# Kernel tuning notes

Hardware: AMD Instinct MI355X
Metric: run time of the kernel (lower is better)

## Reference

```python
import jax, jax.numpy as jnp
import numpy as np

N_NODES = 100000
N_EDGES = 2400000


def setup_inputs() -> dict:
    key = jax.random.key(0)
    ks = jax.random.split(key, 6)
    x = jax.random.normal(ks[0], (N_NODES, 2), dtype=jnp.float32)
    edge_index = jax.random.randint(ks[1], (2, N_EDGES), 0, N_NODES, dtype=jnp.int64)
    # GCNConv weights (glorot-ish scale) and zero biases
    W1 = jax.random.normal(ks[2], (2, 32), dtype=jnp.float32) * (1.0 / np.sqrt(2.0))
    b1 = jnp.zeros((32,), dtype=jnp.float32)
    W2 = jax.random.normal(ks[3], (32, 32), dtype=jnp.float32) * (1.0 / np.sqrt(32.0))
    b2 = jnp.zeros((32,), dtype=jnp.float32)
    W3 = jax.random.normal(ks[4], (32, 1), dtype=jnp.float32) * (1.0 / np.sqrt(32.0))
    b3 = jnp.zeros((1,), dtype=jnp.float32)
    return {"x": x, "edge_index": edge_index, "W1": W1, "b1": b1,
            "W2": W2, "b2": b2, "W3": W3, "b3": b3}


def reference(x, edge_index, W1, b1, W2, b2, W3, b3):
    N = x.shape[0]
    self_loops = jnp.arange(N, dtype=edge_index.dtype)
    src = jnp.concatenate([edge_index[0], self_loops])  # message sources
    dst = jnp.concatenate([edge_index[1], self_loops])  # aggregation targets
    # Symmetric GCN normalization: deg computed at target nodes (PyG gcn_norm)
    deg = jax.ops.segment_sum(jnp.ones_like(dst, dtype=x.dtype), dst, num_segments=N)
    dinv = jnp.where(deg > 0, jax.lax.rsqrt(deg), 0.0)
    norm = (dinv[src] * dinv[dst])[:, None]  # [E+N, 1]

    def gcn_layer(h, W, b):
        h = h @ W                                  # [N, out]
        msg = norm * h[src]                        # gather + scale
        agg = jax.ops.segment_sum(msg, dst, num_segments=N)  # scatter-add
        return agg + b

    h = jax.nn.relu(gcn_layer(x, W1, b1))
    h = jax.nn.relu(gcn_layer(h, W2, b2))
    out = gcn_layer(h, W3, b3)
    return out.reshape(-1)
```

## Files before the change

### kernel.cpp

```cpp
#include <hip/hip_runtime.h>

#define NN 100000
#define NE 2400000
#define NB 391
#define CAP 6912
#define EPB 4096
#define NBLK2 ((NE + EPB - 1) / EPB)

__device__ __forceinline__ int wexscan(int v, int lane) {
    int x = v;
#pragma unroll
    for (int off = 1; off < 64; off <<= 1) {
        int t = __shfl_up(x, off, 64);
        x += (lane >= off) ? t : 0;
    }
    return x - v;
}

__global__ __launch_bounds__(512) void k_hist(const int* __restrict__ ei,
        int* __restrict__ bh) {
    __shared__ int hist[NB];
    int tid = threadIdx.x;
    for (int i = tid; i < NB; i += 512) hist[i] = 0;
    __syncthreads();
    int base_e = blockIdx.x * EPB + tid * 8;
    if (base_e + 8 <= NE) {
        int4 da = *(const int4*)(ei + NE + base_e);
        int4 db = *(const int4*)(ei + NE + base_e + 4);
        atomicAdd(&hist[da.x >> 8], 1); atomicAdd(&hist[da.y >> 8], 1);
        atomicAdd(&hist[da.z >> 8], 1); atomicAdd(&hist[da.w >> 8], 1);
        atomicAdd(&hist[db.x >> 8], 1); atomicAdd(&hist[db.y >> 8], 1);
        atomicAdd(&hist[db.z >> 8], 1); atomicAdd(&hist[db.w >> 8], 1);
    }
    __syncthreads();
    for (int i = tid; i < NB; i += 512) bh[blockIdx.x * NB + i] = hist[i];
}

__global__ __launch_bounds__(256) void k_offscan(int* __restrict__ bh,
        int* __restrict__ tot) {
    __shared__ int wsum[4];
    int b = blockIdx.x, tid = threadIdx.x;
    int lane = tid & 63, wid = tid >> 6;
    int carry = 0;
#pragma unroll
    for (int r = 0; r < 3; ++r) {
        int blk = r * 256 + tid;
        int v = (blk < NBLK2) ? bh[blk * NB + b] : 0;
        int ex = wexscan(v, lane);
        if (lane == 63) wsum[wid] = ex + v;
        __syncthreads();
        int woff = 0, rt = 0;
#pragma unroll
        for (int i = 0; i < 4; ++i) {
            woff += (i < wid) ? wsum[i] : 0;
            rt += wsum[i];
        }
        if (blk < NBLK2) bh[blk * NB + b] = b * CAP + carry + woff + ex;
        carry += rt;
        __syncthreads();
    }
    if (tid == 0) tot[b] = carry;
}

__global__ __launch_bounds__(512) void k_scatter2(const int* __restrict__ ei,
        const int* __restrict__ bh, int* __restrict__ binned) {
    __shared__ int hist[NB], lbase[NB], myb[NB];
    __shared__ int stage[EPB];
    __shared__ unsigned short stageb[EPB];
    __shared__ int wsum[8];
    int tid = threadIdx.x;
    for (int i = tid; i < NB; i += 512) {
        hist[i] = 0;
        myb[i] = bh[blockIdx.x * NB + i];
    }
    __syncthreads();
    int base_e = blockIdx.x * EPB + tid * 8;
    int pk[8], bn[8], rk[8];
    if (base_e + 8 <= NE) {
        const int4* s4 = (const int4*)(ei + base_e);
        const int4* d4 = (const int4*)(ei + NE + base_e);
        int4 sa = s4[0], sb = s4[1], da = d4[0], db = d4[1];
        int ss[8] = {sa.x, sa.y, sa.z, sa.w, sb.x, sb.y, sb.z, sb.w};
        int dd[8] = {da.x, da.y, da.z, da.w, db.x, db.y, db.z, db.w};
#pragma unroll
        for (int k = 0; k < 8; ++k) {
            bn[k] = dd[k] >> 8;
            pk[k] = ss[k] | ((dd[k] & 255) << 17);
            rk[k] = atomicAdd(&hist[bn[k]], 1);
        }
    } else {
#pragma unroll
        for (int k = 0; k < 8; ++k) bn[k] = -1;
    }
    __syncthreads();
    int lane = tid & 63, wid = tid >> 6;
    int v = (tid < NB) ? hist[tid] : 0;
    int ex = wexscan(v, lane);
    if (lane == 63) wsum[wid] = ex + v;
    __syncthreads();
    int woff = 0, tot = 0;
#pragma unroll
    for (int i = 0; i < 8; ++i) {
        int s = wsum[i];
        woff += (i < wid) ? s : 0;
        tot += s;
    }
    ex += woff;
    if (tid < NB) lbase[tid] = ex;
    __syncthreads();
#pragma unroll
    for (int k = 0; k < 8; ++k) {
        if (bn[k] >= 0) {
            int slot = lbase[bn[k]] + rk[k];
            stage[slot] = pk[k];
            stageb[slot] = (unsigned short)bn[k];
        }
    }
    __syncthreads();
    for (int j = tid; j < tot; j += 512) {
        int b = stageb[j];
        binned[myb[b] + (j - lbase[b])] = stage[j];
    }
}

__global__ __launch_bounds__(256) void k_csr_count(const int* __restrict__ binned,
        const int* __restrict__ tot, const float* __restrict__ x,
        int* __restrict__ rsp, float* __restrict__ dinv, float2* __restrict__ xs) {
    __shared__ int cnt[256];
    __shared__ int wsum[4];
    int tid = threadIdx.x, b = blockIdx.x;
    int base = b * CAP, n = tot[b];
    cnt[tid] = 0;
    __syncthreads();
    int n4 = n >> 2;
    const int4* b4 = (const int4*)(binned + base);
    for (int j = tid; j < n4; j += 256) {
        int4 w = b4[j];
        atomicAdd(&cnt[(w.x >> 17) & 255], 1);
        atomicAdd(&cnt[(w.y >> 17) & 255], 1);
        atomicAdd(&cnt[(w.z >> 17) & 255], 1);
        atomicAdd(&cnt[(w.w >> 17) & 255], 1);
    }
    for (int j = (n4 << 2) + tid; j < n; j += 256)
        atomicAdd(&cnt[(binned[base + j] >> 17) & 255], 1);
    __syncthreads();
    int deg = cnt[tid];
    int lane = tid & 63, wid = tid >> 6;
    int ex = wexscan(deg, lane);
    if (lane == 63) wsum[wid] = ex + deg;
    __syncthreads();
    int woff = 0;
#pragma unroll
    for (int i = 0; i < 4; ++i) woff += (i < wid) ? wsum[i] : 0;
    ex += woff;
    int node = (b << 8) + tid;
    if (node < NN) {
        rsp[node] = ((base + ex) << 8) | deg;
        float di = rsqrtf((float)(deg + 1));
        dinv[node] = di;
        float2 xv = ((const float2*)x)[node];
        xs[node] = make_float2(di * xv.x, di * xv.y);
    }
}

__global__ __launch_bounds__(256) void k_csr_place(const int* __restrict__ binned,
        const int* __restrict__ tot, const int* __restrict__ rsp,
        const float2* __restrict__ xs, const float* __restrict__ dinv,
        int* __restrict__ csr, float4* __restrict__ At) {
    __shared__ int cur2[256];
    int tid = threadIdx.x, b = blockIdx.x;
    int base = b * CAP, n = tot[b];
    int node = (b << 8) + tid;
    int rp = (node < NN) ? rsp[node] : 0;
    cur2[tid] = (node < NN) ? ((rp >> 8) - base) : 0;
    __syncthreads();
    int n4 = n >> 2;
    const int4* b4 = (const int4*)(binned + base);
    for (int j = tid; j < n4; j += 256) {
        int4 w = b4[j];
        int p0 = atomicAdd(&cur2[(w.x >> 17) & 255], 1); csr[base + p0] = w.x & 0x1FFFF;
        int p1 = atomicAdd(&cur2[(w.y >> 17) & 255], 1); csr[base + p1] = w.y & 0x1FFFF;
        int p2 = atomicAdd(&cur2[(w.z >> 17) & 255], 1); csr[base + p2] = w.z & 0x1FFFF;
        int p3 = atomicAdd(&cur2[(w.w >> 17) & 255], 1); csr[base + p3] = w.w & 0x1FFFF;
    }
    for (int j = (n4 << 2) + tid; j < n; j += 256) {
        int w = binned[base + j];
        int p = atomicAdd(&cur2[(w >> 17) & 255], 1);
        csr[base + p] = w & 0x1FFFF;
    }
    __syncthreads();
    if (node < NN) {
        int beg = rp >> 8, deg = rp & 255;
        float ax = 0.f, ay = 0.f;
        int e = beg, end = beg + deg;
        for (; e + 4 <= end; e += 4) {
            int s0 = csr[e], s1 = csr[e + 1], s2 = csr[e + 2], s3 = csr[e + 3];
            float2 v0 = xs[s0], v1 = xs[s1], v2 = xs[s2], v3 = xs[s3];
            ax += (v0.x + v1.x) + (v2.x + v3.x);
            ay += (v0.y + v1.y) + (v2.y + v3.y);
        }
        for (; e < end; ++e) { float2 vv = xs[csr[e]]; ax += vv.x; ay += vv.y; }
        float di = dinv[node];
        float2 xn = xs[node];
        At[node] = make_float4(di * (ax + xn.x), di * (ay + xn.y), di, 0.f);
    }
}

__global__ __launch_bounds__(256) void k_agg(const float4* __restrict__ At,
        const int* __restrict__ rsp, const int* __restrict__ csr,
        const float* __restrict__ W1, const float* __restrict__ b1,
        const float* __restrict__ W2, const float* __restrict__ b2,
        const float* __restrict__ W3, float* __restrict__ h3) {
    __shared__ float accS[32 * 36];
    __shared__ float diS[32];
    int tid = threadIdx.x;
    int o = tid & 7, nl = tid >> 3;
    int node = blockIdx.x * 32 + nl;
    int f = tid & 31;

    float4 w0 = *(const float4*)&W1[4 * o];
    float4 w1 = *(const float4*)&W1[32 + 4 * o];
    float4 bb = *(const float4*)&b1[4 * o];

    int r = rsp[node];
    int beg = r >> 8, deg = r & 255;
    float4 an = At[node];
    float di = an.z;

    float4 acc;
    {
        float v0 = fmaf(an.y, w1.x, fmaf(an.x, w0.x, bb.x));
        float v1 = fmaf(an.y, w1.y, fmaf(an.x, w0.y, bb.y));
        float v2 = fmaf(an.y, w1.z, fmaf(an.x, w0.z, bb.z));
        float v3 = fmaf(an.y, w1.w, fmaf(an.x, w0.w, bb.w));
        acc.x = di * fmaxf(v0, 0.f);
        acc.y = di * fmaxf(v1, 0.f);
        acc.z = di * fmaxf(v2, 0.f);
        acc.w = di * fmaxf(v3, 0.f);
    }

    auto acc1 = [&](const float4& aa, float zz) {
        float v0 = fmaf(aa.y, w1.x, fmaf(aa.x, w0.x, bb.x));
        float v1 = fmaf(aa.y, w1.y, fmaf(aa.x, w0.y, bb.y));
        float v2 = fmaf(aa.y, w1.z, fmaf(aa.x, w0.z, bb.z));
        float v3 = fmaf(aa.y, w1.w, fmaf(aa.x, w0.w, bb.w));
        acc.x = fmaf(zz, fmaxf(v0, 0.f), acc.x);
        acc.y = fmaf(zz, fmaxf(v1, 0.f), acc.y);
        acc.z = fmaf(zz, fmaxf(v2, 0.f), acc.z);
        acc.w = fmaf(zz, fmaxf(v3, 0.f), acc.w);
    };

    for (int j = 0; j < deg; j += 4) {
        int e = beg + j;
        int t0 = csr[e];
        int t1 = csr[e + 1], t2 = csr[e + 2], t3 = csr[e + 3];
        int s1 = (j + 1 < deg) ? t1 : 0;
        int s2 = (j + 2 < deg) ? t2 : 0;
        int s3 = (j + 3 < deg) ? t3 : 0;
        float m1 = (j + 1 < deg) ? 1.f : 0.f;
        float m2 = (j + 2 < deg) ? 1.f : 0.f;
        float m3 = (j + 3 < deg) ? 1.f : 0.f;
        float4 a0 = At[t0], a1 = At[s1], a2 = At[s2], a3 = At[s3];
        float z0 = a0.z, z1 = m1 * a1.z, z2 = m2 * a2.z, z3 = m3 * a3.z;
        acc1(a0, z0); acc1(a1, z1); acc1(a2, z2); acc1(a3, z3);
    }

    float w2r[32];
#pragma unroll
    for (int k = 0; k < 32; ++k) w2r[k] = W2[k * 32 + f];

    acc.x *= di; acc.y *= di; acc.z *= di; acc.w *= di;
    *(float4*)&accS[nl * 36 + 4 * o] = acc;
    if (o == 0) diS[nl] = di;
    __syncthreads();

    float bf = b2[f], w3f = W3[f];
    int g = tid >> 5;
#pragma unroll
    for (int rr = 0; rr < 4; ++rr) {
        int n = g + 8 * rr;
        const float* arow = &accS[n * 36];
        float sum = bf;
#pragma unroll
        for (int k = 0; k < 32; k += 4) {
            float4 a4 = *(const float4*)&arow[k];
            sum = fmaf(a4.x, w2r[k], sum);
            sum = fmaf(a4.y, w2r[k + 1], sum);
            sum = fmaf(a4.z, w2r[k + 2], sum);
            sum = fmaf(a4.w, w2r[k + 3], sum);
        }
        float h2 = fmaxf(sum, 0.f);
        float v = h2 * w3f;
#pragma unroll
        for (int off = 16; off > 0; off >>= 1) v += __shfl_down(v, off, 32);
        if (f == 0) h3[blockIdx.x * 32 + n] = diS[n] * v;
    }
}

__global__ __launch_bounds__(256) void k_gather_out(const float* __restrict__ hs,
        const int* __restrict__ rsp, const int* __restrict__ csr,
        const float* __restrict__ dinv, const float* __restrict__ bias,
        float* __restrict__ out) {
    int node = blockIdx.x * 256 + threadIdx.x;
    if (node >= NN) return;
    int r = rsp[node];
    int beg = r >> 8, end = beg + (r & 255);
    float acc = hs[node];
    int e = beg;
    for (; e + 4 <= end; e += 4) {
        int s0 = csr[e], s1 = csr[e + 1], s2 = csr[e + 2], s3 = csr[e + 3];
        acc += (hs[s0] + hs[s1]) + (hs[s2] + hs[s3]);
    }
    for (; e < end; ++e) acc += hs[csr[e]];
    out[node] = dinv[node] * acc + bias[0];
}

extern "C" void kernel_launch(void* const* d_in, const int* in_sizes, int n_in,
                              void* d_out, int out_size, void* d_ws, size_t ws_size,
                              hipStream_t stream) {
    const float* x  = (const float*)d_in[0];
    const int*   ei = (const int*)d_in[1];
    const float* W1 = (const float*)d_in[2];
    const float* b1 = (const float*)d_in[3];
    const float* W2 = (const float*)d_in[4];
    const float* b2 = (const float*)d_in[5];
    const float* W3 = (const float*)d_in[6];
    const float* b3 = (const float*)d_in[7];
    float* out = (float*)d_out;

    char* w = (char*)d_ws;
    float4* At    = (float4*)w; w += NN * 16;
    float2* xs    = (float2*)w; w += NN * 8;
    int*   bh     = (int*)w;    w += NBLK2 * NB * 4;
    int*   tot    = (int*)w;    w += NB * 4;
    int*   rsp    = (int*)w;    w += NN * 4;
    float* dinv   = (float*)w;  w += NN * 4;
    int*   binned = (int*)w;    w += NB * CAP * 4;
    int*   csr    = (int*)w;    w += (NB * CAP + 16) * 4;
    float* h3     = (float*)w;  w += NN * 4;

    const int G_N = (NN + 255) / 256;
    const int G_A = NN / 32;

    k_hist<<<NBLK2, 512, 0, stream>>>(ei, bh);
    k_offscan<<<NB, 256, 0, stream>>>(bh, tot);
    k_scatter2<<<NBLK2, 512, 0, stream>>>(ei, bh, binned);
    k_csr_count<<<NB, 256, 0, stream>>>(binned, tot, x, rsp, dinv, xs);
    k_csr_place<<<NB, 256, 0, stream>>>(binned, tot, rsp, xs, dinv, csr, At);
    k_agg<<<G_A, 256, 0, stream>>>(At, rsp, csr, W1, b1, W2, b2, W3, h3);
    k_gather_out<<<G_N, 256, 0, stream>>>(h3, rsp, csr, dinv, b3, out);
}
```

Measured before the change: 171.2 us.

## Pad CSR rows to multiples of four and pipeline vectorized neighbor gathers

Each CSR row is padded to a multiple of four entries that point at a sentinel node NN, whose features are zeroed in At, xs and h3. This lets the place, aggregate and output kernels read neighbor indices as aligned int4 loads and drop the per-element bounds masks. Each gather loop is also software-pipelined: the next index vector and the next group of feature loads are issued before the current group is accumulated. The cost is larger CSR and feature buffers, a few extra sentinel gathers per row, and index reads that run slightly past each row, which are masked to stay in range.

```diff
diff --git a/kernel.cpp b/kernel.cpp
--- a/kernel.cpp
+++ b/kernel.cpp
@@ -4,8 +4,11 @@
 #define NE 2400000
 #define NB 391
 #define CAP 6912
+#define CAP2 7168
 #define EPB 4096
 #define NBLK2 ((NE + EPB - 1) / EPB)
+#define IMASK 0x1FFFF
+#define SLACK 131072
 
 __device__ __forceinline__ int wexscan(int v, int lane) {
     int x = v;
@@ -145,9 +148,10 @@
         atomicAdd(&cnt[(binned[base + j] >> 17) & 255], 1);
     __syncthreads();
     int deg = cnt[tid];
+    int degp = (deg + 3) & ~3;
     int lane = tid & 63, wid = tid >> 6;
-    int ex = wexscan(deg, lane);
-    if (lane == 63) wsum[wid] = ex + deg;
+    int ex = wexscan(degp, lane);
+    if (lane == 63) wsum[wid] = ex + degp;
     __syncthreads();
     int woff = 0;
 #pragma unroll
@@ -155,12 +159,13 @@
     ex += woff;
     int node = (b << 8) + tid;
     if (node < NN) {
-        rsp[node] = ((base + ex) << 8) | deg;
+        rsp[node] = ((b * CAP2 + ex) << 8) | deg;
         float di = rsqrtf((float)(deg + 1));
         dinv[node] = di;
         float2 xv = ((const float2*)x)[node];
         xs[node] = make_float2(di * xv.x, di * xv.y);
     }
+    if (node == NN) xs[NN] = make_float2(0.f, 0.f);
 }
 
 __global__ __launch_bounds__(256) void k_csr_place(const int* __restrict__ binned,
@@ -169,37 +174,48 @@
         int* __restrict__ csr, float4* __restrict__ At) {
     __shared__ int cur2[256];
     int tid = threadIdx.x, b = blockIdx.x;
-    int base = b * CAP, n = tot[b];
+    int base = b * CAP, base2 = b * CAP2, n = tot[b];
     int node = (b << 8) + tid;
     int rp = (node < NN) ? rsp[node] : 0;
-    cur2[tid] = (node < NN) ? ((rp >> 8) - base) : 0;
+    cur2[tid] = (node < NN) ? ((rp >> 8) - base2) : 0;
     __syncthreads();
     int n4 = n >> 2;
     const int4* b4 = (const int4*)(binned + base);
     for (int j = tid; j < n4; j += 256) {
         int4 w = b4[j];
-        int p0 = atomicAdd(&cur2[(w.x >> 17) & 255], 1); csr[base + p0] = w.x & 0x1FFFF;
-        int p1 = atomicAdd(&cur2[(w.y >> 17) & 255], 1); csr[base + p1] = w.y & 0x1FFFF;
-        int p2 = atomicAdd(&cur2[(w.z >> 17) & 255], 1); csr[base + p2] = w.z & 0x1FFFF;
-        int p3 = atomicAdd(&cur2[(w.w >> 17) & 255], 1); csr[base + p3] = w.w & 0x1FFFF;
+        int p0 = atomicAdd(&cur2[(w.x >> 17) & 255], 1); csr[base2 + p0] = w.x & IMASK;
+        int p1 = atomicAdd(&cur2[(w.y >> 17) & 255], 1); csr[base2 + p1] = w.y & IMASK;
+        int p2 = atomicAdd(&cur2[(w.z >> 17) & 255], 1); csr[base2 + p2] = w.z & IMASK;
+        int p3 = atomicAdd(&cur2[(w.w >> 17) & 255], 1); csr[base2 + p3] = w.w & IMASK;
     }
     for (int j = (n4 << 2) + tid; j < n; j += 256) {
         int w = binned[base + j];
         int p = atomicAdd(&cur2[(w >> 17) & 255], 1);
-        csr[base + p] = w & 0x1FFFF;
-    }
-    __syncthreads();
+        csr[base2 + p] = w & IMASK;
+    }
+    __syncthreads();
+    if (node == NN) At[NN] = make_float4(0.f, 0.f, 0.f, 0.f);
     if (node < NN) {
         int beg = rp >> 8, deg = rp & 255;
+        int degp = (deg + 3) & ~3, nIt = degp >> 2;
+        for (int p = deg; p < degp; ++p) csr[beg + p] = NN;
         float ax = 0.f, ay = 0.f;
-        int e = beg, end = beg + deg;
-        for (; e + 4 <= end; e += 4) {
-            int s0 = csr[e], s1 = csr[e + 1], s2 = csr[e + 2], s3 = csr[e + 3];
-            float2 v0 = xs[s0], v1 = xs[s1], v2 = xs[s2], v3 = xs[s3];
-            ax += (v0.x + v1.x) + (v2.x + v3.x);
-            ay += (v0.y + v1.y) + (v2.y + v3.y);
-        }
-        for (; e < end; ++e) { float2 vv = xs[csr[e]]; ax += vv.x; ay += vv.y; }
+        const int4* cp = (const int4*)(csr + beg);
+        if (nIt > 0) {
+            int4 c1 = cp[1];
+            int4 c0 = cp[0];
+            float2 A0 = xs[c0.x & IMASK], A1 = xs[c0.y & IMASK];
+            float2 A2 = xs[c0.z & IMASK], A3 = xs[c0.w & IMASK];
+            for (int it = 0; it < nIt; ++it) {
+                int4 cn = cp[it + 2];
+                float2 B0 = xs[c1.x & IMASK], B1 = xs[c1.y & IMASK];
+                float2 B2 = xs[c1.z & IMASK], B3 = xs[c1.w & IMASK];
+                ax += (A0.x + A1.x) + (A2.x + A3.x);
+                ay += (A0.y + A1.y) + (A2.y + A3.y);
+                A0 = B0; A1 = B1; A2 = B2; A3 = B3;
+                c1 = cn;
+            }
+        }
         float di = dinv[node];
         float2 xn = xs[node];
         At[node] = make_float4(di * (ax + xn.x), di * (ay + xn.y), di, 0.f);
@@ -214,6 +230,7 @@
     __shared__ float accS[32 * 36];
     __shared__ float diS[32];
     int tid = threadIdx.x;
+    if (blockIdx.x == 0 && tid == 0) h3[NN] = 0.f;
     int o = tid & 7, nl = tid >> 3;
     int node = blockIdx.x * 32 + nl;
     int f = tid & 31;
@@ -224,6 +241,7 @@
 
     int r = rsp[node];
     int beg = r >> 8, deg = r & 255;
+    int degp = (deg + 3) & ~3, nIt = degp >> 2;
     float4 an = At[node];
     float di = an.z;
 
@@ -239,30 +257,30 @@
         acc.w = di * fmaxf(v3, 0.f);
     }
 
-    auto acc1 = [&](const float4& aa, float zz) {
+    auto acc1 = [&](const float4& aa) {
         float v0 = fmaf(aa.y, w1.x, fmaf(aa.x, w0.x, bb.x));
         float v1 = fmaf(aa.y, w1.y, fmaf(aa.x, w0.y, bb.y));
         float v2 = fmaf(aa.y, w1.z, fmaf(aa.x, w0.z, bb.z));
         float v3 = fmaf(aa.y, w1.w, fmaf(aa.x, w0.w, bb.w));
-        acc.x = fmaf(zz, fmaxf(v0, 0.f), acc.x);
-        acc.y = fmaf(zz, fmaxf(v1, 0.f), acc.y);
-        acc.z = fmaf(zz, fmaxf(v2, 0.f), acc.z);
-        acc.w = fmaf(zz, fmaxf(v3, 0.f), acc.w);
+        acc.x = fmaf(aa.z, fmaxf(v0, 0.f), acc.x);
+        acc.y = fmaf(aa.z, fmaxf(v1, 0.f), acc.y);
+        acc.z = fmaf(aa.z, fmaxf(v2, 0.f), acc.z);
+        acc.w = fmaf(aa.z, fmaxf(v3, 0.f), acc.w);
     };
 
-    for (int j = 0; j < deg; j += 4) {
-        int e = beg + j;
-        int t0 = csr[e];
-        int t1 = csr[e + 1], t2 = csr[e + 2], t3 = csr[e + 3];
-        int s1 = (j + 1 < deg) ? t1 : 0;
-        int s2 = (j + 2 < deg) ? t2 : 0;
-        int s3 = (j + 3 < deg) ? t3 : 0;
-        float m1 = (j + 1 < deg) ? 1.f : 0.f;
-        float m2 = (j + 2 < deg) ? 1.f : 0.f;
-        float m3 = (j + 3 < deg) ? 1.f : 0.f;
-        float4 a0 = At[t0], a1 = At[s1], a2 = At[s2], a3 = At[s3];
-        float z0 = a0.z, z1 = m1 * a1.z, z2 = m2 * a2.z, z3 = m3 * a3.z;
-        acc1(a0, z0); acc1(a1, z1); acc1(a2, z2); acc1(a3, z3);
+    const int4* cp = (const int4*)(csr + beg);
+    {
+        int4 c0 = cp[0], c1 = cp[1];
+        float4 A0 = At[c0.x & IMASK], A1 = At[c0.y & IMASK];
+        float4 A2 = At[c0.z & IMASK], A3 = At[c0.w & IMASK];
+        for (int it = 0; it < nIt; ++it) {
+            int4 cn = cp[it + 2];
+            float4 B0 = At[c1.x & IMASK], B1 = At[c1.y & IMASK];
+            float4 B2 = At[c1.z & IMASK], B3 = At[c1.w & IMASK];
+            acc1(A0); acc1(A1); acc1(A2); acc1(A3);
+            A0 = B0; A1 = B1; A2 = B2; A3 = B3;
+            c1 = cn;
+        }
     }
 
     float w2r[32];
@@ -304,14 +322,23 @@
     int node = blockIdx.x * 256 + threadIdx.x;
     if (node >= NN) return;
     int r = rsp[node];
-    int beg = r >> 8, end = beg + (r & 255);
+    int beg = r >> 8, deg = r & 255;
+    int degp = (deg + 3) & ~3, nIt = degp >> 2;
     float acc = hs[node];
-    int e = beg;
-    for (; e + 4 <= end; e += 4) {
-        int s0 = csr[e], s1 = csr[e + 1], s2 = csr[e + 2], s3 = csr[e + 3];
-        acc += (hs[s0] + hs[s1]) + (hs[s2] + hs[s3]);
-    }
-    for (; e < end; ++e) acc += hs[csr[e]];
+    const int4* cp = (const int4*)(csr + beg);
+    if (nIt > 0) {
+        int4 c0 = cp[0], c1 = cp[1];
+        float A0 = hs[c0.x & IMASK], A1 = hs[c0.y & IMASK];
+        float A2 = hs[c0.z & IMASK], A3 = hs[c0.w & IMASK];
+        for (int it = 0; it < nIt; ++it) {
+            int4 cn = cp[it + 2];
+            float B0 = hs[c1.x & IMASK], B1 = hs[c1.y & IMASK];
+            float B2 = hs[c1.z & IMASK], B3 = hs[c1.w & IMASK];
+            acc += (A0 + A1) + (A2 + A3);
+            A0 = B0; A1 = B1; A2 = B2; A3 = B3;
+            c1 = cn;
+        }
+    }
     out[node] = dinv[node] * acc + bias[0];
 }
 
@@ -329,15 +356,15 @@
     float* out = (float*)d_out;
 
     char* w = (char*)d_ws;
-    float4* At    = (float4*)w; w += NN * 16;
-    float2* xs    = (float2*)w; w += NN * 8;
+    float4* At    = (float4*)w; w += SLACK * 16;
+    float2* xs    = (float2*)w; w += SLACK * 8;
     int*   bh     = (int*)w;    w += NBLK2 * NB * 4;
     int*   tot    = (int*)w;    w += NB * 4;
     int*   rsp    = (int*)w;    w += NN * 4;
     float* dinv   = (float*)w;  w += NN * 4;
     int*   binned = (int*)w;    w += NB * CAP * 4;
-    int*   csr    = (int*)w;    w += (NB * CAP + 16) * 4;
-    float* h3     = (float*)w;  w += NN * 4;
+    int*   csr    = (int*)w;    w += (NB * CAP2 + 16) * 4;
+    float* h3     = (float*)w;  w += SLACK * 4;
 
     const int G_N = (NN + 255) / 256;
     const int G_A = NN / 32;
```

Result: no change. 168.4 us (-1.6%).
